# Kernel tuning notes

Hardware: AMD Instinct MI355X
Metric: run time of the kernel (lower is better)

Reference implementation:

```python
import jax, jax.numpy as jnp
import numpy as np

# config
L, G, H, R, S, A, B = 4, 8, 2048, 128, 512, 64, 4096


def setup_inputs() -> dict:
    key = jax.random.key(0)
    ks = jax.random.split(key, 9)
    scale = 0.02
    s = jax.random.normal(ks[0], (B, S), dtype=jnp.float32)
    o = jax.random.randint(ks[1], (B,), 0, G)
    W_in = jax.random.normal(ks[2], (S, H), dtype=jnp.float32) * scale
    b_in = jnp.zeros((H,), jnp.float32)
    W_main = jax.random.normal(ks[3], (L, H, H), dtype=jnp.float32) * scale
    b_main = jnp.zeros((L, H), jnp.float32)
    W_g1 = jax.random.normal(ks[4], (L, G, H, R), dtype=jnp.float32) * scale
    b_g1 = jnp.zeros((L, G, R), jnp.float32)
    W_g2 = jax.random.normal(ks[5], (L, G, R, H), dtype=jnp.float32) * scale
    b_g2 = jnp.zeros((L, G, H), jnp.float32)
    W_out = jax.random.normal(ks[6], (H, A), dtype=jnp.float32) * scale
    b_out = jnp.zeros((A,), jnp.float32)
    return {"s": s, "o": o, "W_in": W_in, "b_in": b_in, "W_main": W_main,
            "b_main": b_main, "W_g1": W_g1, "b_g1": b_g1, "W_g2": W_g2,
            "b_g2": b_g2, "W_out": W_out, "b_out": b_out}


def reference(s, o, W_in, b_in, W_main, b_main, W_g1, b_g1, W_g2, b_g2, W_out, b_out):
    # one-hot routing mask [B, G]; dropout p=0 / eval -> identity
    onehot = jax.nn.one_hot(o, G, dtype=s.dtype)
    x = s @ W_in + b_in  # [B, H]
    for i in range(L):
        main = x @ W_main[i] + b_main[i]  # [B, H]
        # low-rank expert branch: compute all experts' down-proj (small [B,G,R]),
        # mask to the routed expert, then up-project grouped.
        h1 = jnp.einsum('bh,ghr->bgr', x, W_g1[i]) + b_g1[i][None]  # [B,G,R]
        h1m = h1 * onehot[:, :, None]
        g = jnp.einsum('bgr,grh->bh', h1m, W_g2[i]) + onehot @ b_g2[i]  # [B,H]
        x = jax.nn.elu(main + g)
    return x @ W_out + b_out  # logits [B, A]
```

## Files before the change

kernel.cpp:

```cpp
#include <hip/hip_runtime.h>
#include <hip/hip_bf16.h>

#define LL 4
#define GG 8
#define HH 2048
#define RR 128
#define SS 512
#define AOUT 64
#define BBB 4096

typedef __bf16 bf16x8 __attribute__((ext_vector_type(8)));
typedef float f32x4 __attribute__((ext_vector_type(4)));

__device__ __forceinline__ unsigned short f2b(float v) {
    return __builtin_bit_cast(unsigned short, __float2bfloat16(v));
}
__device__ __forceinline__ float b2f(unsigned short u) {
    return __builtin_bit_cast(float, (unsigned)u << 16);
}

__global__ void fix_o_kernel(const int* __restrict__ o_raw, int* __restrict__ e, int B) {
    __shared__ int oddzero, oor;
    if (threadIdx.x == 0) { oddzero = 1; oor = 0; }
    __syncthreads();
    int lodd = 1, loor = 0;
    for (int r = threadIdx.x; r < B; r += 1024) {
        int v = o_raw[r];
        if (r & 1) lodd &= (v == 0);
        if (v < 0 || v >= 8) loor = 1;
    }
    if (!lodd) atomicAnd(&oddzero, 0);
    if (loor) atomicOr(&oor, 1);
    __syncthreads();
    for (int r = threadIdx.x; r < B; r += 1024) {
        int v;
        if (oddzero) v = o_raw[2 * r];
        else if (oor) v = (int)__builtin_bit_cast(float, o_raw[r]);
        else v = o_raw[r];
        e[r] = v & 7;
    }
}

__global__ void cast_bf16_kernel(const float* __restrict__ in,
                                 unsigned short* __restrict__ out, int n) {
    int i = (blockIdx.x * 256 + threadIdx.x) * 4;
    if (i + 3 < n) {
        float4 v = *reinterpret_cast<const float4*>(in + i);
        ushort4 o;
        o.x = f2b(v.x); o.y = f2b(v.y); o.z = f2b(v.z); o.w = f2b(v.w);
        *reinterpret_cast<ushort4*>(out + i) = o;
    }
}

__global__ void tcast_kernel(const float* __restrict__ in,
                             unsigned short* __restrict__ out,
                             int Rr, int Cc, long bsi, long bso) {
    __shared__ float t[32][33];
    const float* src = in + (size_t)blockIdx.z * bsi;
    unsigned short* dst = out + (size_t)blockIdx.z * bso;
    int r0 = blockIdx.y * 32, c0 = blockIdx.x * 32;
    int tx = threadIdx.x, ty = threadIdx.y;
#pragma unroll
    for (int j = 0; j < 4; ++j)
        t[ty + j * 8][tx] = src[(size_t)(r0 + ty + j * 8) * Cc + c0 + tx];
    __syncthreads();
#pragma unroll
    for (int j = 0; j < 4; ++j)
        dst[(size_t)(c0 + ty + j * 8) * Rr + r0 + tx] = f2b(t[tx][ty + j * 8]);
}

template <int EPI>
__global__ __launch_bounds__(256) void gemm_kernel(
    const unsigned short* __restrict__ Ag, const unsigned short* __restrict__ Btg,
    int M, int N, int K,
    const float* __restrict__ bias, const int* __restrict__ eo,
    const float* __restrict__ bias2, const unsigned short* __restrict__ main_in,
    unsigned short* __restrict__ outB) {
    __shared__ __align__(16) unsigned short Alds[128 * 32];
    __shared__ __align__(16) unsigned short Blds[128 * 32];
    const int tid = threadIdx.x;
    const int lane = tid & 63;
    const int wid = tid >> 6;
    const int lo = lane & 15, hi = lane >> 4;
    const int m0 = blockIdx.x * 128, n0 = blockIdx.y * 128;
    const int wm = (wid & 1) * 64, wn = (wid >> 1) * 64;

    f32x4 acc[4][4] = {};

    for (int k0 = 0; k0 < K; k0 += 32) {
#pragma unroll
        for (int t = 0; t < 4; ++t) {
            int c = t * 256 + tid;
            if (c < 512) {
                const unsigned short* g =
                    Ag + (size_t)(m0 + (c >> 2)) * K + k0 + (c & 3) * 8;
                __builtin_amdgcn_global_load_lds(
                    (const __attribute__((address_space(1))) void*)g,
                    (__attribute__((address_space(3))) void*)(Alds + (size_t)c * 8),
                    16, 0, 0);
            } else {
                int d = c - 512;
                const unsigned short* g =
                    Btg + (size_t)(n0 + (d >> 2)) * K + k0 + (d & 3) * 8;
                __builtin_amdgcn_global_load_lds(
                    (const __attribute__((address_space(1))) void*)g,
                    (__attribute__((address_space(3))) void*)(Blds + (size_t)d * 8),
                    16, 0, 0);
            }
        }
        asm volatile("s_waitcnt vmcnt(0)" ::: "memory");
        __syncthreads();

        bf16x8 af[4], bfr[4];
#pragma unroll
        for (int mi = 0; mi < 4; ++mi)
            af[mi] = *reinterpret_cast<const bf16x8*>(
                &Alds[(wm + mi * 16 + lo) * 32 + hi * 8]);
#pragma unroll
        for (int ni = 0; ni < 4; ++ni)
            bfr[ni] = *reinterpret_cast<const bf16x8*>(
                &Blds[(wn + ni * 16 + lo) * 32 + hi * 8]);
#pragma unroll
        for (int mi = 0; mi < 4; ++mi)
#pragma unroll
            for (int ni = 0; ni < 4; ++ni)
                acc[mi][ni] = __builtin_amdgcn_mfma_f32_16x16x32_bf16(
                    af[mi], bfr[ni], acc[mi][ni], 0, 0, 0);
        __syncthreads();
    }

#pragma unroll
    for (int mi = 0; mi < 4; ++mi) {
        const int mrow = m0 + wm + mi * 16 + hi * 4;
#pragma unroll
        for (int ni = 0; ni < 4; ++ni) {
            const int col = n0 + wn + ni * 16 + lo;
            if constexpr (EPI == 0) {
                float bv = bias[col];
#pragma unroll
                for (int r = 0; r < 4; ++r)
                    outB[(size_t)(mrow + r) * N + col] = f2b(acc[mi][ni][r] + bv);
            } else if constexpr (EPI == 2) {
                float bv = bias[col];
                int ce = col >> 7;
#pragma unroll
                for (int r = 0; r < 4; ++r) {
                    float v = ((eo[mrow + r] & 7) == ce) ? (acc[mi][ni][r] + bv)
                                                         : 0.0f;
                    outB[(size_t)(mrow + r) * N + col] = f2b(v);
                }
            } else {
#pragma unroll
                for (int r = 0; r < 4; ++r) {
                    int row = mrow + r;
                    float v = acc[mi][ni][r] +
                              bias2[(size_t)(eo[row] & 7) * N + col] +
                              b2f(main_in[(size_t)row * N + col]);
                    v = v > 0.0f ? v : expm1f(v);
                    outB[(size_t)row * N + col] = f2b(v);
                }
            }
        }
    }
}

__global__ __launch_bounds__(256) void gemm_out_kernel(
    const unsigned short* __restrict__ Ag, const unsigned short* __restrict__ Btg,
    const float* __restrict__ bias, float* __restrict__ outF) {
    __shared__ __align__(16) unsigned short Alds[128 * 32];
    __shared__ __align__(16) unsigned short Blds[64 * 32];
    const int tid = threadIdx.x;
    const int lane = tid & 63;
    const int wid = tid >> 6;
    const int lo = lane & 15, hi = lane >> 4;
    const int m0 = blockIdx.x * 128;
    const int wm = wid * 32;

    f32x4 acc[2][4] = {};

    for (int k0 = 0; k0 < HH; k0 += 32) {
#pragma unroll
        for (int t = 0; t < 2; ++t) {
            int c = t * 256 + tid;
            const unsigned short* g =
                Ag + (size_t)(m0 + (c >> 2)) * HH + k0 + (c & 3) * 8;
            __builtin_amdgcn_global_load_lds(
                (const __attribute__((address_space(1))) void*)g,
                (__attribute__((address_space(3))) void*)(Alds + (size_t)c * 8),
                16, 0, 0);
        }
        {
            const unsigned short* g =
                Btg + (size_t)(tid >> 2) * HH + k0 + (tid & 3) * 8;
            __builtin_amdgcn_global_load_lds(
                (const __attribute__((address_space(1))) void*)g,
                (__attribute__((address_space(3))) void*)(Blds + (size_t)tid * 8),
                16, 0, 0);
        }
        asm volatile("s_waitcnt vmcnt(0)" ::: "memory");
        __syncthreads();

        bf16x8 af[2], bfr[4];
#pragma unroll
        for (int mi = 0; mi < 2; ++mi)
            af[mi] = *reinterpret_cast<const bf16x8*>(
                &Alds[(wm + mi * 16 + lo) * 32 + hi * 8]);
#pragma unroll
        for (int ni = 0; ni < 4; ++ni)
            bfr[ni] = *reinterpret_cast<const bf16x8*>(
                &Blds[(ni * 16 + lo) * 32 + hi * 8]);
#pragma unroll
        for (int mi = 0; mi < 2; ++mi)
#pragma unroll
            for (int ni = 0; ni < 4; ++ni)
                acc[mi][ni] = __builtin_amdgcn_mfma_f32_16x16x32_bf16(
                    af[mi], bfr[ni], acc[mi][ni], 0, 0, 0);
        __syncthreads();
    }

#pragma unroll
    for (int mi = 0; mi < 2; ++mi) {
        const int mrow = m0 + wm + mi * 16 + hi * 4;
#pragma unroll
        for (int ni = 0; ni < 4; ++ni) {
            const int col = ni * 16 + lo;
            float bv = bias[col];
#pragma unroll
            for (int r = 0; r < 4; ++r)
                outF[(size_t)(mrow + r) * AOUT + col] = acc[mi][ni][r] + bv;
        }
    }
}

extern "C" void kernel_launch(void* const* d_in, const int* in_sizes, int n_in,
                              void* d_out, int out_size, void* d_ws, size_t ws_size,
                              hipStream_t stream) {
    const float* s      = (const float*)d_in[0];
    const int*   o_raw  = (const int*)d_in[1];
    const float* W_in   = (const float*)d_in[2];
    const float* b_in   = (const float*)d_in[3];
    const float* W_main = (const float*)d_in[4];
    const float* b_main = (const float*)d_in[5];
    const float* W_g1   = (const float*)d_in[6];
    const float* b_g1   = (const float*)d_in[7];
    const float* W_g2   = (const float*)d_in[8];
    const float* b_g2   = (const float*)d_in[9];
    const float* W_out  = (const float*)d_in[10];
    const float* b_out  = (const float*)d_in[11];
    (void)in_sizes; (void)n_in; (void)out_size;

    char* ws = (char*)d_ws;
    size_t off = 0;
    auto alloc = [&](size_t bytes) {
        void* p = ws + off;
        off += (bytes + 255) & ~(size_t)255;
        return p;
    };
    int*            e     = (int*)alloc(65536);
    unsigned short* X     = (unsigned short*)alloc((size_t)BBB * HH * 2);
    unsigned short* Wt    = (unsigned short*)alloc((size_t)HH * HH * 2);
    unsigned short* sbuf  = (unsigned short*)alloc((size_t)BBB * GG * RR * 2);
    unsigned short* mainb = (unsigned short*)alloc((size_t)BBB * HH * 2);
    if (ws_size < off) return;

    dim3 tb(32, 8);

    fix_o_kernel<<<1, 1024, 0, stream>>>(o_raw, e, BBB);

    cast_bf16_kernel<<<BBB * SS / 1024, 256, 0, stream>>>(s, sbuf, BBB * SS);
    tcast_kernel<<<dim3(HH / 32, SS / 32, 1), tb, 0, stream>>>(W_in, Wt, SS, HH, 0, 0);
    gemm_kernel<0><<<dim3(BBB / 128, HH / 128), 256, 0, stream>>>(
        sbuf, Wt, BBB, HH, SS, b_in, nullptr, nullptr, nullptr, X);

    for (int i = 0; i < LL; ++i) {
        tcast_kernel<<<dim3(HH / 32, HH / 32, 1), tb, 0, stream>>>(
            W_main + (size_t)i * HH * HH, Wt, HH, HH, 0, 0);
        gemm_kernel<0><<<dim3(BBB / 128, HH / 128), 256, 0, stream>>>(
            X, Wt, BBB, HH, HH, b_main + i * HH, nullptr, nullptr, nullptr, mainb);
        tcast_kernel<<<dim3(RR / 32, HH / 32, GG), tb, 0, stream>>>(
            W_g1 + (size_t)i * GG * HH * RR, Wt, HH, RR, (long)HH * RR,
            (long)RR * HH);
        gemm_kernel<2><<<dim3(BBB / 128, GG * RR / 128), 256, 0, stream>>>(
            X, Wt, BBB, GG * RR, HH, b_g1 + i * GG * RR, e, nullptr, nullptr, sbuf);
        tcast_kernel<<<dim3(HH / 32, GG * RR / 32, 1), tb, 0, stream>>>(
            W_g2 + (size_t)i * GG * RR * HH, Wt, GG * RR, HH, 0, 0);
        gemm_kernel<3><<<dim3(BBB / 128, HH / 128), 256, 0, stream>>>(
            sbuf, Wt, BBB, HH, GG * RR, nullptr, e, b_g2 + (size_t)i * GG * HH,
            mainb, X);
    }

    tcast_kernel<<<dim3(AOUT / 32, HH / 32, 1), tb, 0, stream>>>(W_out, Wt, HH,
                                                                AOUT, 0, 0);
    gemm_out_kernel<<<BBB / 128, 256, 0, stream>>>(X, Wt, b_out, (float*)d_out);
}
```

Before: 817.4 us.

## Double-buffer LDS in GEMMs and fuse main and expert down-projection GEMMs

Result: faster. 668.7 us (-18.2%).

```diff
diff --git a/kernel.cpp b/kernel.cpp
--- a/kernel.cpp
+++ b/kernel.cpp
@@ -73,21 +73,24 @@
 __global__ __launch_bounds__(256) void gemm_kernel(
     const unsigned short* __restrict__ Ag, const unsigned short* __restrict__ Btg,
     int M, int N, int K,
-    const float* __restrict__ bias, const int* __restrict__ eo,
-    const float* __restrict__ bias2, const unsigned short* __restrict__ main_in,
-    unsigned short* __restrict__ outB) {
-    __shared__ __align__(16) unsigned short Alds[128 * 32];
-    __shared__ __align__(16) unsigned short Blds[128 * 32];
+    const float* __restrict__ bias, const float* __restrict__ biasg,
+    const int* __restrict__ eo, const float* __restrict__ bias2,
+    const unsigned short* __restrict__ main_in,
+    unsigned short* __restrict__ outB, unsigned short* __restrict__ outB2) {
+    __shared__ __align__(16) unsigned short Alds[2][128 * 32];
+    __shared__ __align__(16) unsigned short Blds[2][128 * 32];
     const int tid = threadIdx.x;
     const int lane = tid & 63;
     const int wid = tid >> 6;
     const int lo = lane & 15, hi = lane >> 4;
     const int m0 = blockIdx.x * 128, n0 = blockIdx.y * 128;
     const int wm = (wid & 1) * 64, wn = (wid >> 1) * 64;
+    const int NT = K >> 5;
 
     f32x4 acc[4][4] = {};
 
-    for (int k0 = 0; k0 < K; k0 += 32) {
+    auto STAGE = [&](int b, int kt) {
+        const int k0 = kt << 5;
 #pragma unroll
         for (int t = 0; t < 4; ++t) {
             int c = t * 256 + tid;
@@ -96,7 +99,7 @@
                     Ag + (size_t)(m0 + (c >> 2)) * K + k0 + (c & 3) * 8;
                 __builtin_amdgcn_global_load_lds(
                     (const __attribute__((address_space(1))) void*)g,
-                    (__attribute__((address_space(3))) void*)(Alds + (size_t)c * 8),
+                    (__attribute__((address_space(3))) void*)(&Alds[b][c * 8]),
                     16, 0, 0);
             } else {
                 int d = c - 512;
@@ -104,29 +107,39 @@
                     Btg + (size_t)(n0 + (d >> 2)) * K + k0 + (d & 3) * 8;
                 __builtin_amdgcn_global_load_lds(
                     (const __attribute__((address_space(1))) void*)g,
-                    (__attribute__((address_space(3))) void*)(Blds + (size_t)d * 8),
+                    (__attribute__((address_space(3))) void*)(&Blds[b][d * 8]),
                     16, 0, 0);
             }
         }
-        asm volatile("s_waitcnt vmcnt(0)" ::: "memory");
-        __syncthreads();
+    };
+
+    STAGE(0, 0);
+    asm volatile("s_waitcnt vmcnt(0)" ::: "memory");
+    __syncthreads();
+
+    int cur = 0;
+    for (int kt = 0; kt < NT; ++kt) {
+        if (kt + 1 < NT) STAGE(cur ^ 1, kt + 1);
 
         bf16x8 af[4], bfr[4];
 #pragma unroll
         for (int mi = 0; mi < 4; ++mi)
             af[mi] = *reinterpret_cast<const bf16x8*>(
-                &Alds[(wm + mi * 16 + lo) * 32 + hi * 8]);
+                &Alds[cur][(wm + mi * 16 + lo) * 32 + hi * 8]);
 #pragma unroll
         for (int ni = 0; ni < 4; ++ni)
             bfr[ni] = *reinterpret_cast<const bf16x8*>(
-                &Blds[(wn + ni * 16 + lo) * 32 + hi * 8]);
+                &Blds[cur][(wn + ni * 16 + lo) * 32 + hi * 8]);
 #pragma unroll
         for (int mi = 0; mi < 4; ++mi)
 #pragma unroll
             for (int ni = 0; ni < 4; ++ni)
                 acc[mi][ni] = __builtin_amdgcn_mfma_f32_16x16x32_bf16(
                     af[mi], bfr[ni], acc[mi][ni], 0, 0, 0);
+
+        asm volatile("s_waitcnt vmcnt(0)" ::: "memory");
         __syncthreads();
+        cur ^= 1;
     }
 
 #pragma unroll
@@ -140,16 +153,7 @@
 #pragma unroll
                 for (int r = 0; r < 4; ++r)
                     outB[(size_t)(mrow + r) * N + col] = f2b(acc[mi][ni][r] + bv);
-            } else if constexpr (EPI == 2) {
-                float bv = bias[col];
-                int ce = col >> 7;
-#pragma unroll
-                for (int r = 0; r < 4; ++r) {
-                    float v = ((eo[mrow + r] & 7) == ce) ? (acc[mi][ni][r] + bv)
-                                                         : 0.0f;
-                    outB[(size_t)(mrow + r) * N + col] = f2b(v);
-                }
-            } else {
+            } else if constexpr (EPI == 3) {
 #pragma unroll
                 for (int r = 0; r < 4; ++r) {
                     int row = mrow + r;
@@ -159,6 +163,24 @@
                     v = v > 0.0f ? v : expm1f(v);
                     outB[(size_t)row * N + col] = f2b(v);
                 }
+            } else {
+                if (n0 < HH) {
+                    float bv = bias[col];
+#pragma unroll
+                    for (int r = 0; r < 4; ++r)
+                        outB[(size_t)(mrow + r) * HH + col] =
+                            f2b(acc[mi][ni][r] + bv);
+                } else {
+                    int hc = col - HH;
+                    int ce = hc >> 7;
+                    float bv = biasg[hc];
+#pragma unroll
+                    for (int r = 0; r < 4; ++r) {
+                        float v = ((eo[mrow + r] & 7) == ce)
+                                      ? (acc[mi][ni][r] + bv) : 0.0f;
+                        outB2[(size_t)(mrow + r) * (GG * RR) + hc] = f2b(v);
+                    }
+                }
             }
         }
     }
@@ -167,68 +189,63 @@
 __global__ __launch_bounds__(256) void gemm_out_kernel(
     const unsigned short* __restrict__ Ag, const unsigned short* __restrict__ Btg,
     const float* __restrict__ bias, float* __restrict__ outF) {
-    __shared__ __align__(16) unsigned short Alds[128 * 32];
-    __shared__ __align__(16) unsigned short Blds[64 * 32];
+    __shared__ __align__(16) unsigned short Alds[2][64 * 32];
+    __shared__ __align__(16) unsigned short Blds[2][64 * 32];
     const int tid = threadIdx.x;
     const int lane = tid & 63;
     const int wid = tid >> 6;
     const int lo = lane & 15, hi = lane >> 4;
-    const int m0 = blockIdx.x * 128;
-    const int wm = wid * 32;
-
-    f32x4 acc[2][4] = {};
-
-    for (int k0 = 0; k0 < HH; k0 += 32) {
-#pragma unroll
-        for (int t = 0; t < 2; ++t) {
-            int c = t * 256 + tid;
-            const unsigned short* g =
-                Ag + (size_t)(m0 + (c >> 2)) * HH + k0 + (c & 3) * 8;
-            __builtin_amdgcn_global_load_lds(
-                (const __attribute__((address_space(1))) void*)g,
-                (__attribute__((address_space(3))) void*)(Alds + (size_t)c * 8),
-                16, 0, 0);
-        }
-        {
-            const unsigned short* g =
-                Btg + (size_t)(tid >> 2) * HH + k0 + (tid & 3) * 8;
-            __builtin_amdgcn_global_load_lds(
-                (const __attribute__((address_space(1))) void*)g,
-                (__attribute__((address_space(3))) void*)(Blds + (size_t)tid * 8),
-                16, 0, 0);
-        }
+    const int m0 = blockIdx.x * 64;
+    const int wm = wid * 16;
+    const int NT = HH >> 5;
+
+    f32x4 acc[4] = {};
+
+    auto STAGE = [&](int b, int kt) {
+        const int k0 = kt << 5;
+        const int c = tid;
+        const unsigned short* ga =
+            Ag + (size_t)(m0 + (c >> 2)) * HH + k0 + (c & 3) * 8;
+        __builtin_amdgcn_global_load_lds(
+            (const __attribute__((address_space(1))) void*)ga,
+            (__attribute__((address_space(3))) void*)(&Alds[b][c * 8]), 16, 0, 0);
+        const unsigned short* gb =
+            Btg + (size_t)(c >> 2) * HH + k0 + (c & 3) * 8;
+        __builtin_amdgcn_global_load_lds(
+            (const __attribute__((address_space(1))) void*)gb,
+            (__attribute__((address_space(3))) void*)(&Blds[b][c * 8]), 16, 0, 0);
+    };
+
+    STAGE(0, 0);
+    asm volatile("s_waitcnt vmcnt(0)" ::: "memory");
+    __syncthreads();
+
+    int cur = 0;
+    for (int kt = 0; kt < NT; ++kt) {
+        if (kt + 1 < NT) STAGE(cur ^ 1, kt + 1);
+        bf16x8 af = *reinterpret_cast<const bf16x8*>(
+            &Alds[cur][(wm + lo) * 32 + hi * 8]);
+        bf16x8 bfr[4];
+#pragma unroll
+        for (int ni = 0; ni < 4; ++ni)
+            bfr[ni] = *reinterpret_cast<const bf16x8*>(
+                &Blds[cur][(ni * 16 + lo) * 32 + hi * 8]);
+#pragma unroll
+        for (int ni = 0; ni < 4; ++ni)
+            acc[ni] = __builtin_amdgcn_mfma_f32_16x16x32_bf16(af, bfr[ni],
+                                                              acc[ni], 0, 0, 0);
         asm volatile("s_waitcnt vmcnt(0)" ::: "memory");
         __syncthreads();
-
-        bf16x8 af[2], bfr[4];
-#pragma unroll
-        for (int mi = 0; mi < 2; ++mi)
-            af[mi] = *reinterpret_cast<const bf16x8*>(
-                &Alds[(wm + mi * 16 + lo) * 32 + hi * 8]);
-#pragma unroll
-        for (int ni = 0; ni < 4; ++ni)
-            bfr[ni] = *reinterpret_cast<const bf16x8*>(
-                &Blds[(ni * 16 + lo) * 32 + hi * 8]);
-#pragma unroll
-        for (int mi = 0; mi < 2; ++mi)
-#pragma unroll
-            for (int ni = 0; ni < 4; ++ni)
-                acc[mi][ni] = __builtin_amdgcn_mfma_f32_16x16x32_bf16(
-                    af[mi], bfr[ni], acc[mi][ni], 0, 0, 0);
-        __syncthreads();
-    }
-
-#pragma unroll
-    for (int mi = 0; mi < 2; ++mi) {
-        const int mrow = m0 + wm + mi * 16 + hi * 4;
-#pragma unroll
-        for (int ni = 0; ni < 4; ++ni) {
-            const int col = ni * 16 + lo;
-            float bv = bias[col];
-#pragma unroll
-            for (int r = 0; r < 4; ++r)
-                outF[(size_t)(mrow + r) * AOUT + col] = acc[mi][ni][r] + bv;
-        }
+        cur ^= 1;
+    }
+
+#pragma unroll
+    for (int ni = 0; ni < 4; ++ni) {
+        const int col = ni * 16 + lo;
+        float bv = bias[col];
+#pragma unroll
+        for (int r = 0; r < 4; ++r)
+            outF[(size_t)(m0 + wm + hi * 4 + r) * AOUT + col] = acc[ni][r] + bv;
     }
 }
 
@@ -258,7 +275,7 @@
     };
     int*            e     = (int*)alloc(65536);
     unsigned short* X     = (unsigned short*)alloc((size_t)BBB * HH * 2);
-    unsigned short* Wt    = (unsigned short*)alloc((size_t)HH * HH * 2);
+    unsigned short* Wt    = (unsigned short*)alloc((size_t)(HH + GG * RR) * HH * 2);
     unsigned short* sbuf  = (unsigned short*)alloc((size_t)BBB * GG * RR * 2);
     unsigned short* mainb = (unsigned short*)alloc((size_t)BBB * HH * 2);
     if (ws_size < off) return;
@@ -270,26 +287,25 @@
     cast_bf16_kernel<<<BBB * SS / 1024, 256, 0, stream>>>(s, sbuf, BBB * SS);
     tcast_kernel<<<dim3(HH / 32, SS / 32, 1), tb, 0, stream>>>(W_in, Wt, SS, HH, 0, 0);
     gemm_kernel<0><<<dim3(BBB / 128, HH / 128), 256, 0, stream>>>(
-        sbuf, Wt, BBB, HH, SS, b_in, nullptr, nullptr, nullptr, X);
+        sbuf, Wt, BBB, HH, SS, b_in, nullptr, nullptr, nullptr, nullptr, X, nullptr);
 
     for (int i = 0; i < LL; ++i) {
         tcast_kernel<<<dim3(HH / 32, HH / 32, 1), tb, 0, stream>>>(
             W_main + (size_t)i * HH * HH, Wt, HH, HH, 0, 0);
-        gemm_kernel<0><<<dim3(BBB / 128, HH / 128), 256, 0, stream>>>(
-            X, Wt, BBB, HH, HH, b_main + i * HH, nullptr, nullptr, nullptr, mainb);
         tcast_kernel<<<dim3(RR / 32, HH / 32, GG), tb, 0, stream>>>(
-            W_g1 + (size_t)i * GG * HH * RR, Wt, HH, RR, (long)HH * RR,
-            (long)RR * HH);
-        gemm_kernel<2><<<dim3(BBB / 128, GG * RR / 128), 256, 0, stream>>>(
-            X, Wt, BBB, GG * RR, HH, b_g1 + i * GG * RR, e, nullptr, nullptr, sbuf);
+            W_g1 + (size_t)i * GG * HH * RR, Wt + (size_t)HH * HH, HH, RR,
+            (long)HH * RR, (long)RR * HH);
+        gemm_kernel<4><<<dim3(BBB / 128, (HH + GG * RR) / 128), 256, 0, stream>>>(
+            X, Wt, BBB, HH + GG * RR, HH, b_main + i * HH, b_g1 + i * GG * RR,
+            e, nullptr, nullptr, mainb, sbuf);
         tcast_kernel<<<dim3(HH / 32, GG * RR / 32, 1), tb, 0, stream>>>(
             W_g2 + (size_t)i * GG * RR * HH, Wt, GG * RR, HH, 0, 0);
         gemm_kernel<3><<<dim3(BBB / 128, HH / 128), 256, 0, stream>>>(
-            sbuf, Wt, BBB, HH, GG * RR, nullptr, e, b_g2 + (size_t)i * GG * HH,
-            mainb, X);
+            sbuf, Wt, BBB, HH, GG * RR, nullptr, nullptr, e,
+            b_g2 + (size_t)i * GG * HH, mainb, X, nullptr);
     }
 
     tcast_kernel<<<dim3(AOUT / 32, HH / 32, 1), tb, 0, stream>>>(W_out, Wt, HH,
                                                                 AOUT, 0, 0);
-    gemm_out_kernel<<<BBB / 128, 256, 0, stream>>>(X, Wt, b_out, (float*)d_out);
-}
+    gemm_out_kernel<<<BBB / 64, 256, 0, stream>>>(X, Wt, b_out, (float*)d_out);
+}
```
